# Optimization experiments

Measured on AMD Instinct MI355X. Metric: run time of the kernel, lower is better.

Reference implementation:

```python
import math
import jax
import jax.numpy as jnp
from jax import lax
import numpy as np

LARGE_NUMBER = 1e10
NEG = -1e30  # finite stand-in for -inf (safe for logaddexp grads)
K = 64
TRAIN_ENSEMBLE = 2


def _init_esp(M, k, dtype):
    # log elementary symmetric polys of the empty set: e_0 = 1, e_r>0 = 0
    return jnp.full((M, k + 1), NEG, dtype).at[:, 0].set(0.0)


def _esp_step(carry, th_col):
    # carry: [M, k+1] log e_r; add one item with logit th_col: e_r <- e_r + w*e_{r-1}
    M = carry.shape[0]
    shifted = jnp.concatenate([jnp.full((M, 1), NEG, carry.dtype), carry[:, :-1]], axis=1)
    new = jnp.logaddexp(carry, shifted + th_col[:, None])
    return new, new


def log_ek_sum(theta, k):
    # sum over rows of log e_k(exp(theta_row)); grad wrt theta = exact-k inclusion marginals
    init = _init_esp(theta.shape[0], k, theta.dtype)
    final, _ = lax.scan(lambda c, t: (_esp_step(c, t)[0], None), init, theta.T)
    return final[:, k].sum()


def marginals_exact_k(theta, k):
    return jax.grad(lambda th: log_ek_sum(th, k))(theta)  # [M, N]


def suffix_esp_table(theta, k):
    # T[j] = log elem. symmetric polys of suffix items j..N-1; shape [N+1, M, k+1]
    init = _init_esp(theta.shape[0], k, theta.dtype)
    _, Ts = lax.scan(_esp_step, init, jnp.flip(theta.T, 0))
    return jnp.flip(jnp.concatenate([init[None], Ts], 0), 0)


def sample_exact_k(theta, k, u):
    # sequential conditional sampling of an exact-k subset (conditional Poisson)
    # theta: [M, N], u: [T, M, N] uniforms -> binary samples [T, M, N]
    M, N = theta.shape
    T = u.shape[0]
    Tab = suffix_esp_table(theta, k)  # [N+1, M, k+1]
    ar = jnp.arange(M)

    def step(r, xs):
        th_col, Tc, Tn, u_col = xs  # [M], [M,k+1], [M,k+1], [T,M]
        num = Tn[ar[None, :], jnp.maximum(r - 1, 0)]  # [T, M]
        den = Tc[ar[None, :], r]
        p = jnp.where(r > 0, jnp.exp(th_col[None, :] + num - den), 0.0)
        inc = (u_col < p)
        return r - inc.astype(r.dtype), inc.astype(theta.dtype)

    r0 = jnp.full((T, M), k, jnp.int32)
    _, incs = lax.scan(step, r0, (theta.T, Tab[:-1], Tab[1:], jnp.moveaxis(u, 2, 0)))
    return jnp.moveaxis(incs, 0, 2)  # [T, M, N]


def setup_inputs():
    key = jax.random.key(0)
    k1, k2 = jax.random.split(key)
    scores = jax.random.normal(k1, (64, 4096, 2), jnp.float32)
    u = jax.random.uniform(k2, (TRAIN_ENSEMBLE, 64 * 2, 4096), jnp.float32)
    return {"scores": scores, "u": u}


def reference(scores, u):
    B, Nmax, E = scores.shape
    times_sampled = TRAIN_ENSEMBLE
    local_k = min(K, Nmax)
    flat = scores.transpose(0, 2, 1).reshape(B * E, Nmax)
    N = 2 ** math.ceil(math.log2(Nmax))
    flat = jnp.pad(flat, ((0, 0), (0, N - Nmax)), constant_values=-LARGE_NUMBER)
    marg = marginals_exact_k(flat, local_k)           # [M, N]
    samples = sample_exact_k(flat, local_k, u)        # [T, M, N]
    # straight-through estimator
    samples = lax.stop_gradient(samples - marg[None]) + marg[None]
    samples = samples[..., :Nmax]
    marg = marg[:, :Nmax]
    new_mask = samples.reshape(times_sampled, B, E, Nmax).transpose(0, 1, 3, 2)
    new_marginals = marg.reshape(B, E, Nmax).transpose(0, 2, 1)
    return new_mask, new_marginals
```

## Files before the change

### kernel.cpp

```cpp
#include <hip/hip_runtime.h>
#include <hip/hip_bf16.h>

#define NROWS 128
#define NCOLS 4096
#define KVAL  64
#define NEGV  (-1e30f)
#define LOG2E 1.4426950408889634f
#define LN2   0.6931471805599453f

__device__ float g_suf[(size_t)NROWS * (NCOLS + 1) * 64];
__device__ float g_pre[(size_t)NROWS * (NCOLS + 1) * 64];
__device__ unsigned long long g_mask[(size_t)2 * NROWS * NCOLS];
__device__ unsigned char g_map  [(size_t)2 * NROWS * 64 * 64];
__device__ unsigned char g_entry[(size_t)2 * NROWS * 64];
__device__ unsigned long long g_incs[(size_t)2 * NROWS * 64 * 64];

__device__ __forceinline__ float shr1z(float x) {
    int r = __builtin_amdgcn_update_dpp(0, __float_as_int(x), 0x138, 0xF, 0xF, true);
    return __int_as_float(r);
}
__device__ __forceinline__ float readlane_f(float v, int lane) {
    return __int_as_float(__builtin_amdgcn_readlane(__float_as_int(v), lane));
}
__device__ __forceinline__ float lae_fast(float a, float b) {
    float mx = fmaxf(a, b);
    float d  = fabsf(a - b);
    float e  = __builtin_amdgcn_exp2f(d * -LOG2E);
    return fmaf(__builtin_amdgcn_logf(1.0f + e), LN2, mx);
}

__device__ __forceinline__ float dpp_sum64(float x) {
#define SSTEP(ctrl, rmask) { int t_ = __builtin_amdgcn_update_dpp(0, \
        __float_as_int(x), ctrl, rmask, 0xF, false); x = x + __int_as_float(t_); }
    SSTEP(0x111, 0xF) SSTEP(0x112, 0xF) SSTEP(0x114, 0xF) SSTEP(0x118, 0xF)
    SSTEP(0x142, 0xA) SSTEP(0x143, 0xC)
#undef SSTEP
    return readlane_f(x, 63);
}

__global__ __launch_bounds__(64, 1) void dp_kernel(const float* __restrict__ scores) {
    int blk = blockIdx.x;
    int l = threadIdx.x;
    bool suf = (blk < NROWS);
    int m = suf ? blk : (blk - NROWS);
    float* __restrict__ tab = (suf ? g_suf : g_pre) + (size_t)m * (NCOLS + 1) * 64;
    const float* __restrict__ srow = scores + (size_t)(m >> 1) * (NCOLS * 2) + (m & 1);

    tab[(size_t)(suf ? NCOLS : 0) * 64 + l] = NEGV;
    float s = NEGV;
    if (suf) {
        float tile = srow[(size_t)(NCOLS - 64 + l) * 2];
        for (int t0 = NCOLS - 64; t0 >= 0; t0 -= 64) {
            float nxt = (t0 >= 64) ? srow[(size_t)(t0 - 64 + l) * 2] : 0.0f;
            #pragma unroll
            for (int ss = 63; ss >= 0; --ss) {
                float tht = readlane_f(tile, ss);
                float b = shr1z(s) + tht;
                s = lae_fast(s, b);
                tab[(size_t)(t0 + ss) * 64 + l] = s;
            }
            tile = nxt;
        }
    } else {
        float tile = srow[(size_t)l * 2];
        for (int t0 = 0; t0 < NCOLS; t0 += 64) {
            float nxt = (t0 + 64 < NCOLS) ? srow[(size_t)(t0 + 64 + l) * 2] : 0.0f;
            #pragma unroll
            for (int ss = 0; ss < 64; ++ss) {
                float tht = readlane_f(tile, ss);
                float b = shr1z(s) + tht;
                s = lae_fast(s, b);
                tab[(size_t)(t0 + ss + 1) * 64 + l] = s;
            }
            tile = nxt;
        }
    }
}

__global__ __launch_bounds__(256) void maskA_kernel(const float* __restrict__ scores,
                                                    const float* __restrict__ u,
                                                    float* __restrict__ out) {
    int l = threadIdx.x & 63;
    int wid = threadIdx.x >> 6;
    int unit = blockIdx.x * 4 + wid;
    int m  = unit >> 6;
    int b  = unit & 63;
    int t0 = b << 6;
    size_t rowbase = (size_t)m * (NCOLS + 1) * 64;
    const float* __restrict__ S = g_suf + rowbase;
    const float* __restrict__ P = g_pre + rowbase;
    const float* __restrict__ srow = scores + (size_t)(m >> 1) * (NCOLS * 2) + (m & 1);
    const float* __restrict__ u0 = u + (size_t)m * NCOLS;
    const float* __restrict__ u1 = u + (size_t)(NROWS + m) * NCOLS;

    float thtile = srow[(size_t)(t0 + l) * 2];
    float u0tile = u0[t0 + l];
    float u1tile = u1[t0 + l];

    float den_full = P[(size_t)NCOLS * 64 + 63];

    int pidx = (l < 63) ? (62 - l) : 62;
    float pring[16];
    #pragma unroll
    for (int j = 0; j < 16; ++j)
        pring[j] = P[(size_t)(t0 + j) * 64 + pidx];

    float Dcur = S[(size_t)t0 * 64 + l];
    float sring[16];
    #pragma unroll
    for (int j = 0; j < 16; ++j)
        sring[j] = S[(size_t)(t0 + 1 + j) * 64 + l];

    unsigned long long acc0 = 0, acc1 = 0;
    float mres = 0.0f;
    #pragma unroll
    for (int ss = 0; ss < 64; ++ss) {
        int t = t0 + ss;
        float Dnext = sring[ss & 15];
        int snext = t0 + ss + 17;
        if (snext > t0 + 64) snext = t0 + 64;
        sring[ss & 15] = S[(size_t)snext * 64 + l];
        float num = shr1z(Dnext);
        float den = Dcur;
        float tht = readlane_f(thtile, ss);
        float uu0 = readlane_f(u0tile, ss);
        float uu1 = readlane_f(u1tile, ss);
        float p = __builtin_amdgcn_exp2f(((num + tht) - den) * LOG2E);
        unsigned long long b0 = __ballot(uu0 < p);
        unsigned long long b1 = __ballot(uu1 < p);
        acc0 = (l == ss) ? b0 : acc0;
        acc1 = (l == ss) ? b1 : acc1;
        float vP = (l == 63) ? 0.0f : pring[ss & 15];
        int inext = t + 16;
        if (inext > t0 + 63) inext = t0 + 63;
        pring[ss & 15] = P[(size_t)inext * 64 + pidx];
        float term = __builtin_amdgcn_exp2f((vP + num + (tht - den_full)) * LOG2E);
        float mg = dpp_sum64(term);
        mres = (l == ss) ? mg : mres;
        Dcur = Dnext;
    }
    g_mask[(size_t)m * NCOLS + t0 + l] = acc0;
    g_mask[(size_t)(NROWS + m) * NCOLS + t0 + l] = acc1;
    size_t obase = (size_t)2 * 64 * NCOLS * 2;
    out[obase + ((size_t)(m >> 1) * NCOLS + (t0 + l)) * 2 + (m & 1)] = mres;

    unsigned int a0lo = (unsigned int)acc0, a0hi = (unsigned int)(acc0 >> 32);
    unsigned int a1lo = (unsigned int)acc1, a1hi = (unsigned int)(acc1 >> 32);
    int r0 = l + 1, r1 = l + 1;
    unsigned long long bits0 = 0, bits1 = 0;
    #pragma unroll
    for (int ss = 0; ss < 64; ++ss) {
        unsigned int m0lo = (unsigned int)__builtin_amdgcn_readlane((int)a0lo, ss);
        unsigned int m0hi = (unsigned int)__builtin_amdgcn_readlane((int)a0hi, ss);
        unsigned int m1lo = (unsigned int)__builtin_amdgcn_readlane((int)a1lo, ss);
        unsigned int m1hi = (unsigned int)__builtin_amdgcn_readlane((int)a1hi, ss);
        unsigned long long msk0 = ((unsigned long long)m0hi << 32) | m0lo;
        unsigned long long msk1 = ((unsigned long long)m1hi << 32) | m1lo;
        int inc0 = (r0 > 0) ? (int)((msk0 >> (r0 - 1)) & 1ULL) : 0;
        int inc1 = (r1 > 0) ? (int)((msk1 >> (r1 - 1)) & 1ULL) : 0;
        bits0 |= ((unsigned long long)inc0) << ss;
        bits1 |= ((unsigned long long)inc1) << ss;
        r0 -= inc0;
        r1 -= inc1;
    }
    g_map[((size_t)m * 64 + b) * 64 + l] = (unsigned char)r0;
    g_map[((size_t)(NROWS + m) * 64 + b) * 64 + l] = (unsigned char)r1;
    g_incs[((size_t)m * 64 + b) * 64 + l] = bits0;
    g_incs[((size_t)(NROWS + m) * 64 + b) * 64 + l] = bits1;
}

__global__ __launch_bounds__(256) void scanB_kernel() {
    int c = threadIdx.x;
    int r = KVAL;
    for (int b = 0; b < 64; ++b) {
        g_entry[(size_t)c * 64 + b] = (unsigned char)r;
        int idx = (r > 0) ? (r - 1) : 0;
        int nxt = g_map[((size_t)c * 64 + b) * 64 + idx];
        r = (r > 0) ? nxt : 0;
    }
}

__global__ __launch_bounds__(256) void scanC_kernel(float* __restrict__ out) {
    int l = threadIdx.x & 63;
    int wid = threadIdx.x >> 6;
    int unit = blockIdx.x * 4 + wid;
    int c = unit >> 6;
    int b = unit & 63;
    int tens = c >> 7;
    int m = c & (NROWS - 1);
    float* __restrict__ orow = out + (((size_t)tens * 64 + (m >> 1)) * NCOLS) * 2 + (m & 1);

    int r = g_entry[(size_t)c * 64 + b];
    unsigned long long incvec = (r > 0)
        ? g_incs[((size_t)c * 64 + b) * 64 + (r - 1)] : 0ULL;
    orow[(size_t)(b * 64 + l) * 2] = (float)((incvec >> l) & 1ULL);
}

extern "C" void kernel_launch(void* const* d_in, const int* in_sizes, int n_in,
                              void* d_out, int out_size, void* d_ws, size_t ws_size,
                              hipStream_t stream) {
    const float* scores = (const float*)d_in[0];
    const float* u      = (const float*)d_in[1];
    float* out = (float*)d_out;

    dp_kernel<<<2 * NROWS, 64, 0, stream>>>(scores);
    maskA_kernel<<<2048, 256, 0, stream>>>(scores, u, out);
    scanB_kernel<<<1, 256, 0, stream>>>();
    scanC_kernel<<<4096, 256, 0, stream>>>(out);
}
```

Baseline: 241.0 us.

## Fuse block-chain scan and output expansion into one per-row kernel

Merges the serial single-block chain scan (scanB) and the scatter kernel (scanC) into one kernel with one wavefront per sampled row. The block-to-block rank map is transposed so each lane holds one entry-rank's 64 byte-values in registers, and the chain is walked with readlane lookups instead of 64 dependent global loads per thread. The unused g_mask stores and the g_entry buffer are removed. The cost targeted is the latency-bound single-block scan and one extra launch; each wave in exchange does a serial 64-step readlane chain and then writes 4096 outputs.

After: 219.3 us. 1.1x faster.

```diff
diff --git a/kernel.cpp b/kernel.cpp
--- a/kernel.cpp
+++ b/kernel.cpp
@@ -10,9 +10,7 @@
 
 __device__ float g_suf[(size_t)NROWS * (NCOLS + 1) * 64];
 __device__ float g_pre[(size_t)NROWS * (NCOLS + 1) * 64];
-__device__ unsigned long long g_mask[(size_t)2 * NROWS * NCOLS];
-__device__ unsigned char g_map  [(size_t)2 * NROWS * 64 * 64];
-__device__ unsigned char g_entry[(size_t)2 * NROWS * 64];
+__device__ unsigned char g_map [(size_t)2 * NROWS * 64 * 64];
 __device__ unsigned long long g_incs[(size_t)2 * NROWS * 64 * 64];
 
 __device__ __forceinline__ float shr1z(float x) {
@@ -139,8 +137,6 @@
         mres = (l == ss) ? mg : mres;
         Dcur = Dnext;
     }
-    g_mask[(size_t)m * NCOLS + t0 + l] = acc0;
-    g_mask[(size_t)(NROWS + m) * NCOLS + t0 + l] = acc1;
     size_t obase = (size_t)2 * 64 * NCOLS * 2;
     out[obase + ((size_t)(m >> 1) * NCOLS + (t0 + l)) * 2 + (m & 1)] = mres;
 
@@ -163,37 +159,53 @@
         r0 -= inc0;
         r1 -= inc1;
     }
-    g_map[((size_t)m * 64 + b) * 64 + l] = (unsigned char)r0;
-    g_map[((size_t)(NROWS + m) * 64 + b) * 64 + l] = (unsigned char)r1;
+    g_map[(size_t)m * 4096 + (size_t)l * 64 + b] = (unsigned char)r0;
+    g_map[(size_t)(NROWS + m) * 4096 + (size_t)l * 64 + b] = (unsigned char)r1;
     g_incs[((size_t)m * 64 + b) * 64 + l] = bits0;
     g_incs[((size_t)(NROWS + m) * 64 + b) * 64 + l] = bits1;
 }
 
-__global__ __launch_bounds__(256) void scanB_kernel() {
-    int c = threadIdx.x;
-    int r = KVAL;
-    for (int b = 0; b < 64; ++b) {
-        g_entry[(size_t)c * 64 + b] = (unsigned char)r;
-        int idx = (r > 0) ? (r - 1) : 0;
-        int nxt = g_map[((size_t)c * 64 + b) * 64 + idx];
-        r = (r > 0) ? nxt : 0;
-    }
-}
-
-__global__ __launch_bounds__(256) void scanC_kernel(float* __restrict__ out) {
-    int l = threadIdx.x & 63;
-    int wid = threadIdx.x >> 6;
-    int unit = blockIdx.x * 4 + wid;
-    int c = unit >> 6;
-    int b = unit & 63;
+__global__ __launch_bounds__(64) void scanBC_kernel(float* __restrict__ out) {
+    int c = blockIdx.x;
+    int l = threadIdx.x;
     int tens = c >> 7;
     int m = c & (NROWS - 1);
     float* __restrict__ orow = out + (((size_t)tens * 64 + (m >> 1)) * NCOLS) * 2 + (m & 1);
 
-    int r = g_entry[(size_t)c * 64 + b];
-    unsigned long long incvec = (r > 0)
-        ? g_incs[((size_t)c * 64 + b) * 64 + (r - 1)] : 0ULL;
-    orow[(size_t)(b * 64 + l) * 2] = (float)((incvec >> l) & 1ULL);
+    const uint4* __restrict__ vp =
+        (const uint4*)(g_map + (size_t)c * 4096 + (size_t)l * 64);
+    unsigned int v[16];
+    {
+        uint4 q0 = vp[0], q1 = vp[1], q2 = vp[2], q3 = vp[3];
+        v[0]=q0.x; v[1]=q0.y; v[2]=q0.z; v[3]=q0.w;
+        v[4]=q1.x; v[5]=q1.y; v[6]=q1.z; v[7]=q1.w;
+        v[8]=q2.x; v[9]=q2.y; v[10]=q2.z; v[11]=q2.w;
+        v[12]=q3.x; v[13]=q3.y; v[14]=q3.z; v[15]=q3.w;
+    }
+
+    int r = KVAL;
+    int rvec = 0;
+    #pragma unroll
+    for (int b = 0; b < 64; ++b) {
+        rvec = (l == b) ? r : rvec;
+        int safe = (r > 0) ? (r - 1) : 0;
+        unsigned int word = (unsigned int)__builtin_amdgcn_readlane((int)v[b >> 2], safe);
+        int nxt = (int)((word >> ((b & 3) * 8)) & 0xFFu);
+        r = (r > 0) ? nxt : 0;
+    }
+
+    int e = (rvec > 0) ? (rvec - 1) : 0;
+    unsigned long long iv = g_incs[((size_t)c * 64 + l) * 64 + e];
+    if (rvec == 0) iv = 0ULL;
+    unsigned int ivlo = (unsigned int)iv, ivhi = (unsigned int)(iv >> 32);
+
+    #pragma unroll
+    for (int b = 0; b < 64; ++b) {
+        unsigned int lo = (unsigned int)__builtin_amdgcn_readlane((int)ivlo, b);
+        unsigned int hi = (unsigned int)__builtin_amdgcn_readlane((int)ivhi, b);
+        unsigned long long vec = ((unsigned long long)hi << 32) | lo;
+        orow[(size_t)(b * 64 + l) * 2] = (float)((vec >> l) & 1ULL);
+    }
 }
 
 extern "C" void kernel_launch(void* const* d_in, const int* in_sizes, int n_in,
@@ -205,6 +217,5 @@
 
     dp_kernel<<<2 * NROWS, 64, 0, stream>>>(scores);
     maskA_kernel<<<2048, 256, 0, stream>>>(scores, u, out);
-    scanB_kernel<<<1, 256, 0, stream>>>();
-    scanC_kernel<<<4096, 256, 0, stream>>>(out);
-}
+    scanBC_kernel<<<2 * NROWS, 64, 0, stream>>>(out);
+}
```
